# Kernel optimization log

Hardware: AMD Instinct MI355X
Metric: run time of the kernel (lower is better)

## Reference

```python
import jax, jax.numpy as jnp
import numpy as np

I, H, O = 64, 512, 64
B, S = 32, 2048


def setup_inputs() -> dict:
    key = jax.random.key(0)
    ks = jax.random.split(key, 8)
    def xavier(k, shape):
        fan_in, fan_out = shape[1], shape[0]
        lim = jnp.sqrt(6.0 / (fan_in + fan_out))
        return jax.random.uniform(k, shape, jnp.float32, -lim, lim)
    return {
        "x": jax.random.normal(ks[0], (B, S, I), jnp.float32),
        "h_0": jnp.zeros((B, H), jnp.float32),
        "Wz": xavier(ks[1], (H, I + H)),
        "Wr": xavier(ks[2], (H, I + H)),
        "Wh": xavier(ks[3], (H, I + H)),
        "bz": jnp.ones((H,), jnp.float32),
        "br": jnp.zeros((H,), jnp.float32),
        "bh": jnp.zeros((H,), jnp.float32),
        "W1": xavier(ks[4], (H, H)),
        "b1": jnp.zeros((H,), jnp.float32),
        "W2": xavier(ks[5], (O, H)),
        "b2": jnp.zeros((O,), jnp.float32),
    }


def reference(x, h_0, Wz, Wr, Wh, bz, br, bh, W1, b1, W2, b2):
    def step(h_prev, x_t):
        combined = jnp.concatenate([x_t, h_prev], axis=1)          # [B, I+H]
        z = jax.nn.sigmoid(combined @ Wz.T + bz)                   # [B, H]
        r = jax.nn.sigmoid(combined @ Wr.T + br)                   # [B, H]
        gate_input = jnp.concatenate([r * h_prev, x_t], axis=1)    # [B, H+I]
        h_hat = jnp.tanh(gate_input @ Wh.T + bh)                   # [B, H]
        h_t = (1.0 - z) * h_prev + z * h_hat
        out = jax.nn.relu(h_t @ W1.T + b1) @ W2.T + b2             # [B, O]
        return h_t, out

    # scan over time: x -> [S, B, I]
    h_last, outs = jax.lax.scan(step, h_0, jnp.swapaxes(x, 0, 1))
    return jnp.swapaxes(outs, 0, 1), h_last  # [B, S, O], [B, H]
```

## Files before the change

kernel.cpp:

```cpp
#include <hip/hip_runtime.h>
#include <stdint.h>

#define S_LEN 2048
#define NW 16
#define KPAD 584

typedef __attribute__((ext_vector_type(8))) short short8;
typedef __attribute__((ext_vector_type(4))) float f32x4;

__device__ __forceinline__ unsigned short f2bf(float f) {
  union { float f; unsigned int u; } v; v.f = f;
  unsigned int u = v.u;
  u = (u + 0x7FFFu + ((u >> 16) & 1u)) >> 16;
  return (unsigned short)u;
}

__device__ __forceinline__ float sigm(float x) { return 1.f / (1.f + __expf(-x)); }
__device__ __forceinline__ float tanh_f(float x) {
  float e = __expf(2.f * x);
  return 1.f - 2.f / (e + 1.f);
}

__device__ __forceinline__ void group_barrier(unsigned int* p, unsigned int target) {
  __syncthreads();
  if (threadIdx.x == 0) {
    __threadfence();
    __hip_atomic_fetch_add(p, 1u, __ATOMIC_RELEASE, __HIP_MEMORY_SCOPE_AGENT);
    unsigned int it = 0;
    while (__hip_atomic_load(p, __ATOMIC_RELAXED, __HIP_MEMORY_SCOPE_AGENT) < target) {
      __builtin_amdgcn_s_sleep(1);
      if (++it > (1u << 22)) break;
    }
    __threadfence();
  }
  __syncthreads();
}

__global__ void prep_kernel(const float* __restrict__ Wz, const float* __restrict__ Wr,
                            const float* __restrict__ Wh, const float* __restrict__ W1,
                            const float* __restrict__ W2,
                            unsigned short* __restrict__ WgT,
                            unsigned short* __restrict__ W1T,
                            unsigned short* __restrict__ W2T) {
  const int total = 1536 * 576 + 512 * 512 + 64 * 512;
  for (int idx = blockIdx.x * 256 + threadIdx.x; idx < total; idx += gridDim.x * 256) {
    if (idx < 1536 * 576) {
      int row = idx / 576, k = idx % 576;
      float v;
      if (row < 512)       v = Wz[row * 576 + k];
      else if (row < 1024) v = Wr[(row - 512) * 576 + k];
      else {
        int r = row - 1024;
        v = (k < 64) ? Wh[r * 576 + 512 + k] : Wh[r * 576 + (k - 64)];
      }
      WgT[idx] = f2bf(v);
    } else if (idx < 1536 * 576 + 512 * 512) {
      int i = idx - 1536 * 576;
      W1T[i] = f2bf(W1[i]);
    } else {
      int i = idx - 1536 * 576 - 512 * 512;
      W2T[i] = f2bf(W2[i]);
    }
  }
}

__global__ void __launch_bounds__(256, 1) recur_kernel(
    const float* __restrict__ x, const float* __restrict__ h0,
    const float* __restrict__ bz, const float* __restrict__ br,
    const float* __restrict__ bh, const unsigned short* __restrict__ WgT,
    unsigned short* __restrict__ hbuf, unsigned short* __restrict__ rhbuf,
    unsigned short* __restrict__ h_all, float* __restrict__ h_last,
    unsigned int* __restrict__ ctr) {
  extern __shared__ char smem[];
  unsigned short* Wlds = (unsigned short*)smem;
  unsigned short* Abuf = Wlds + 96 * KPAD;
  float* hfp = (float*)(Abuf + 16 * KPAD);

  const int wg = blockIdx.x;
  const int g = wg >> 4;
  const int w = wg & 15;
  const int tid = threadIdx.x;
  const int lane = tid & 63;
  const int wave = tid >> 6;
  const int crow = (lane >> 4) << 2;
  const int ccol = lane & 15;

  for (int i = tid; i < 96 * 72; i += 256) {
    int lr = i / 72, c = i % 72;
    int gate = lr >> 5, col = lr & 31;
    const uint4* src = (const uint4*)(WgT + (size_t)(gate * 512 + w * 32 + col) * 576);
    *(uint4*)(Wlds + lr * KPAD + c * 8) = src[c];
  }
  for (int i = tid; i < 16 * 32; i += 256) {
    int m = i >> 5, c = i & 31;
    hfp[m * 32 + c] = h0[(size_t)(g * 16 + m) * 512 + w * 32 + c];
  }
  __syncthreads();

  unsigned int* myctr = ctr + g * 4096;
  float zreg[4];

  for (int t = 0; t < S_LEN; ++t) {
    {
      int i = tid;
      int m = i >> 4, c4 = i & 15;
      float4 xv = *(const float4*)(x + ((size_t)(g * 16 + m) * S_LEN + t) * 64 + c4 * 4);
      unsigned short* d = Abuf + m * KPAD + c4 * 4;
      d[0] = f2bf(xv.x); d[1] = f2bf(xv.y); d[2] = f2bf(xv.z); d[3] = f2bf(xv.w);
    }
    if (t == 0) {
      for (int i = tid; i < 16 * 128; i += 256) {
        int m = i >> 7, c4 = i & 127;
        float4 hv = *(const float4*)(h0 + (size_t)(g * 16 + m) * 512 + c4 * 4);
        unsigned short* d = Abuf + m * KPAD + 64 + c4 * 4;
        d[0] = f2bf(hv.x); d[1] = f2bf(hv.y); d[2] = f2bf(hv.z); d[3] = f2bf(hv.w);
      }
    } else {
      for (int i = tid; i < 16 * 64; i += 256) {
        int m = i >> 6, c8 = i & 63;
        uint4 v = *(const uint4*)(hbuf + (size_t)(g * 16 + m) * 512 + c8 * 8);
        *(uint4*)(Abuf + m * KPAD + 64 + c8 * 8) = v;
      }
    }
    __syncthreads();

    {
      const int gsel = wave >> 1;
      const int tile = wave & 1;
      const unsigned short* Ap = Abuf + ccol * KPAD + ((lane >> 4) << 3);
      const unsigned short* Bp = Wlds + (gsel * 32 + tile * 16 + ccol) * KPAD + ((lane >> 4) << 3);
      f32x4 acc = {0.f, 0.f, 0.f, 0.f};
#pragma unroll
      for (int kk = 0; kk < 18; ++kk) {
        short8 a = *(const short8*)(Ap + kk * 32);
        short8 b = *(const short8*)(Bp + kk * 32);
        acc = __builtin_amdgcn_mfma_f32_16x16x32_bf16(a, b, acc, 0, 0, 0);
      }
      const int nloc = tile * 16 + ccol;
      const int ng = w * 32 + nloc;
      const float bias = (gsel == 0) ? bz[ng] : br[ng];
      if (gsel == 0) {
#pragma unroll
        for (int j = 0; j < 4; ++j) zreg[j] = sigm(acc[j] + bias);
      } else {
#pragma unroll
        for (int j = 0; j < 4; ++j) {
          int m = crow + j;
          float rv = sigm(acc[j] + bias);
          float rh = rv * hfp[m * 32 + nloc];
          rhbuf[(size_t)(g * 16 + m) * 512 + ng] = f2bf(rh);
        }
      }
    }
    group_barrier(myctr + t * 2, NW);

    for (int i = tid; i < 16 * 64; i += 256) {
      int m = i >> 6, c8 = i & 63;
      uint4 v = *(const uint4*)(rhbuf + (size_t)(g * 16 + m) * 512 + c8 * 8);
      *(uint4*)(Abuf + m * KPAD + 64 + c8 * 8) = v;
    }
    __syncthreads();

    if (wave < 2) {
      const unsigned short* Ap = Abuf + ccol * KPAD + ((lane >> 4) << 3);
      const unsigned short* Bp = Wlds + (64 + wave * 16 + ccol) * KPAD + ((lane >> 4) << 3);
      f32x4 acc = {0.f, 0.f, 0.f, 0.f};
#pragma unroll
      for (int kk = 0; kk < 18; ++kk) {
        short8 a = *(const short8*)(Ap + kk * 32);
        short8 b = *(const short8*)(Bp + kk * 32);
        acc = __builtin_amdgcn_mfma_f32_16x16x32_bf16(a, b, acc, 0, 0, 0);
      }
      const int nloc = wave * 16 + ccol;
      const int ng = w * 32 + nloc;
      const float bias = bh[ng];
#pragma unroll
      for (int j = 0; j < 4; ++j) {
        int m = crow + j;
        float hh = tanh_f(acc[j] + bias);
        float hold = hfp[m * 32 + nloc];
        float z = zreg[j];
        float hn = (1.f - z) * hold + z * hh;
        hfp[m * 32 + nloc] = hn;
        unsigned short hb = f2bf(hn);
        hbuf[(size_t)(g * 16 + m) * 512 + ng] = hb;
        h_all[((size_t)(g * 16 + m) * S_LEN + t) * 512 + ng] = hb;
        if (t == S_LEN - 1) h_last[(size_t)(g * 16 + m) * 512 + ng] = hn;
      }
    }
    group_barrier(myctr + t * 2 + 1, NW);
  }
}

__global__ void __launch_bounds__(256, 1) head_kernel(
    const unsigned short* __restrict__ h_all, const unsigned short* __restrict__ W1T,
    const unsigned short* __restrict__ W2T, const float* __restrict__ b1,
    const float* __restrict__ b2, float* __restrict__ out) {
  extern __shared__ char smem[];
  unsigned short* hs = (unsigned short*)smem;
  unsigned short* act = hs + 64 * 520;

  const int tid = threadIdx.x, lane = tid & 63, wave = tid >> 6;
  const int crow = (lane >> 4) << 2, ccol = lane & 15;
  const size_t row0 = (size_t)blockIdx.x * 64;

  for (int i = tid; i < 64 * 64; i += 256) {
    int r = i >> 6, c8 = i & 63;
    uint4 v = *(const uint4*)(h_all + (row0 + r) * 512 + c8 * 8);
    *(uint4*)(hs + r * 520 + c8 * 8) = v;
  }
  __syncthreads();

  f32x4 acc[8][4];
#pragma unroll
  for (int nt = 0; nt < 8; ++nt)
#pragma unroll
    for (int mt = 0; mt < 4; ++mt) acc[nt][mt] = {0.f, 0.f, 0.f, 0.f};

  for (int k = 0; k < 16; ++k) {
    short8 a[4];
#pragma unroll
    for (int mt = 0; mt < 4; ++mt)
      a[mt] = *(const short8*)(hs + (mt * 16 + ccol) * 520 + k * 32 + ((lane >> 4) << 3));
#pragma unroll
    for (int nt = 0; nt < 8; ++nt) {
      int n0 = (wave * 8 + nt) * 16;
      short8 b = *(const short8*)(W1T + (size_t)(n0 + ccol) * 512 + k * 32 + ((lane >> 4) << 3));
#pragma unroll
      for (int mt = 0; mt < 4; ++mt)
        acc[nt][mt] = __builtin_amdgcn_mfma_f32_16x16x32_bf16(a[mt], b, acc[nt][mt], 0, 0, 0);
    }
  }
#pragma unroll
  for (int nt = 0; nt < 8; ++nt) {
    int n = wave * 128 + nt * 16 + ccol;
    float bias = b1[n];
#pragma unroll
    for (int mt = 0; mt < 4; ++mt)
#pragma unroll
      for (int j = 0; j < 4; ++j) {
        float v = fmaxf(acc[nt][mt][j] + bias, 0.f);
        act[(mt * 16 + crow + j) * 520 + n] = f2bf(v);
      }
  }
  __syncthreads();
  for (int i = tid; i < 64 * 64; i += 256) {
    int r = i >> 6, c8 = i & 63;
    uint4 v = *(const uint4*)(W2T + (size_t)r * 512 + c8 * 8);
    *(uint4*)(hs + r * 520 + c8 * 8) = v;
  }
  __syncthreads();

  f32x4 acc2[4];
#pragma unroll
  for (int nt = 0; nt < 4; ++nt) acc2[nt] = {0.f, 0.f, 0.f, 0.f};
  for (int k = 0; k < 16; ++k) {
    short8 a = *(const short8*)(act + (wave * 16 + ccol) * 520 + k * 32 + ((lane >> 4) << 3));
#pragma unroll
    for (int nt = 0; nt < 4; ++nt) {
      short8 b = *(const short8*)(hs + (nt * 16 + ccol) * 520 + k * 32 + ((lane >> 4) << 3));
      acc2[nt] = __builtin_amdgcn_mfma_f32_16x16x32_bf16(a, b, acc2[nt], 0, 0, 0);
    }
  }
#pragma unroll
  for (int nt = 0; nt < 4; ++nt) {
    int o = nt * 16 + ccol;
    float bias = b2[o];
#pragma unroll
    for (int j = 0; j < 4; ++j) {
      int r = wave * 16 + crow + j;
      out[(row0 + r) * 64 + o] = acc2[nt][j] + bias;
    }
  }
}

extern "C" void kernel_launch(void* const* d_in, const int* in_sizes, int n_in,
                              void* d_out, int out_size, void* d_ws, size_t ws_size,
                              hipStream_t stream) {
  const float* x  = (const float*)d_in[0];
  const float* h0 = (const float*)d_in[1];
  const float* Wz = (const float*)d_in[2];
  const float* Wr = (const float*)d_in[3];
  const float* Wh = (const float*)d_in[4];
  const float* bz = (const float*)d_in[5];
  const float* br = (const float*)d_in[6];
  const float* bh = (const float*)d_in[7];
  const float* W1 = (const float*)d_in[8];
  const float* b1 = (const float*)d_in[9];
  const float* W2 = (const float*)d_in[10];
  const float* b2 = (const float*)d_in[11];

  char* ws = (char*)d_ws;
  size_t off = 0;
  unsigned int*   ctr   = (unsigned int*)(ws + off);   off += 32768;
  unsigned short* hbuf  = (unsigned short*)(ws + off); off += 32 * 512 * 2;
  unsigned short* rhbuf = (unsigned short*)(ws + off); off += 32 * 512 * 2;
  unsigned short* WgT   = (unsigned short*)(ws + off); off += (size_t)1536 * 576 * 2;
  unsigned short* W1T   = (unsigned short*)(ws + off); off += (size_t)512 * 512 * 2;
  unsigned short* W2T   = (unsigned short*)(ws + off); off += (size_t)64 * 512 * 2;
  unsigned short* h_all = (unsigned short*)(ws + off); off += (size_t)32 * 2048 * 512 * 2;

  float* out = (float*)d_out;
  float* h_last = out + (size_t)32 * 2048 * 64;

  hipMemsetAsync(ctr, 0, 32768, stream);
  hipLaunchKernelGGL(prep_kernel, dim3(1024), dim3(256), 0, stream,
                     Wz, Wr, Wh, W1, W2, WgT, W1T, W2T);

  const int recur_lds = (96 * KPAD + 16 * KPAD) * 2 + 16 * 32 * 4;
  hipFuncSetAttribute(reinterpret_cast<const void*>(&recur_kernel),
                      hipFuncAttributeMaxDynamicSharedMemorySize, recur_lds);
  hipLaunchKernelGGL(recur_kernel, dim3(32), dim3(256), recur_lds, stream,
                     x, h0, bz, br, bh, WgT, hbuf, rhbuf, h_all, h_last, ctr);

  const int head_lds = 2 * 64 * 520 * 2;
  hipFuncSetAttribute(reinterpret_cast<const void*>(&head_kernel),
                      hipFuncAttributeMaxDynamicSharedMemorySize, head_lds);
  hipLaunchKernelGGL(head_kernel, dim3(1024), dim3(256), head_lds, stream,
                     h_all, W1T, W2T, b1, b2, out);
}
```

Measured before the change: 19.34 ms.

## Replace atomic-counter barriers with per-workgroup flags and direct global operand loads

The recurrent kernel's group barrier (atomic add, fence, sleep-poll) becomes per-workgroup monotonic flags that one wave polls with a wave-wide all-check, without sleeps or heavy fences. The h and r*h operands are read straight from global memory into registers via relaxed agent-scope atomic loads instead of being staged through LDS. Weights are pre-swizzled into MFMA fragment order in LDS, x for the next step is prefetched and converted during the current step, and the MFMA chain is split into two accumulators. The aim is to cut per-step synchronisation latency on the serial 2048-step critical path. The price is relying on relaxed atomics without explicit fences for cross-workgroup visibility, which is a memory-ordering risk.

```diff
diff --git a/kernel.cpp b/kernel.cpp
--- a/kernel.cpp
+++ b/kernel.cpp
@@ -2,9 +2,8 @@
 #include <stdint.h>
 
 #define S_LEN 2048
-#define NW 16
-#define KPAD 584
-
+
+typedef unsigned long long u64;
 typedef __attribute__((ext_vector_type(8))) short short8;
 typedef __attribute__((ext_vector_type(4))) float f32x4;
 
@@ -15,25 +14,11 @@
   return (unsigned short)u;
 }
 
-__device__ __forceinline__ float sigm(float x) { return 1.f / (1.f + __expf(-x)); }
-__device__ __forceinline__ float tanh_f(float x) {
-  float e = __expf(2.f * x);
-  return 1.f - 2.f / (e + 1.f);
-}
-
-__device__ __forceinline__ void group_barrier(unsigned int* p, unsigned int target) {
-  __syncthreads();
-  if (threadIdx.x == 0) {
-    __threadfence();
-    __hip_atomic_fetch_add(p, 1u, __ATOMIC_RELEASE, __HIP_MEMORY_SCOPE_AGENT);
-    unsigned int it = 0;
-    while (__hip_atomic_load(p, __ATOMIC_RELAXED, __HIP_MEMORY_SCOPE_AGENT) < target) {
-      __builtin_amdgcn_s_sleep(1);
-      if (++it > (1u << 22)) break;
-    }
-    __threadfence();
-  }
-  __syncthreads();
+__device__ __forceinline__ void st_bf(unsigned short* p, unsigned short v) {
+  __hip_atomic_store(p, v, __ATOMIC_RELAXED, __HIP_MEMORY_SCOPE_AGENT);
+}
+__device__ __forceinline__ u64 ld_u64(const unsigned short* p) {
+  return __hip_atomic_load((const u64*)p, __ATOMIC_RELAXED, __HIP_MEMORY_SCOPE_AGENT);
 }
 
 __global__ void prep_kernel(const float* __restrict__ Wz, const float* __restrict__ Wr,
@@ -70,125 +55,170 @@
     const float* __restrict__ bh, const unsigned short* __restrict__ WgT,
     unsigned short* __restrict__ hbuf, unsigned short* __restrict__ rhbuf,
     unsigned short* __restrict__ h_all, float* __restrict__ h_last,
-    unsigned int* __restrict__ ctr) {
+    unsigned int* __restrict__ flags) {
   extern __shared__ char smem[];
-  unsigned short* Wlds = (unsigned short*)smem;
-  unsigned short* Abuf = Wlds + 96 * KPAD;
-  float* hfp = (float*)(Abuf + 16 * KPAD);
+  unsigned short* Wf = (unsigned short*)smem;
+  unsigned short* Xf = Wf + 6 * 18 * 64 * 8;
+  float* hfp = (float*)(Xf + 2 * 64 * 8);
 
   const int wg = blockIdx.x;
-  const int g = wg >> 4;
-  const int w = wg & 15;
+  const int g = wg >> 4, w = wg & 15;
   const int tid = threadIdx.x;
-  const int lane = tid & 63;
-  const int wave = tid >> 6;
+  const int lane = tid & 63, wave = tid >> 6;
   const int crow = (lane >> 4) << 2;
   const int ccol = lane & 15;
-
-  for (int i = tid; i < 96 * 72; i += 256) {
-    int lr = i / 72, c = i % 72;
-    int gate = lr >> 5, col = lr & 31;
-    const uint4* src = (const uint4*)(WgT + (size_t)(gate * 512 + w * 32 + col) * 576);
-    *(uint4*)(Wlds + lr * KPAD + c * 8) = src[c];
-  }
-  for (int i = tid; i < 16 * 32; i += 256) {
+  const int ko8 = (lane >> 4) << 3;
+
+  for (int i = tid; i < 6 * 18 * 64; i += 256) {
+    int T = i / (18 * 64);
+    int kk = (i >> 6) % 18;
+    int l = i & 63;
+    int row = (T >> 1) * 512 + w * 32 + (T & 1) * 16 + (l & 15);
+    int k = kk * 32 + ((l >> 4) << 3);
+    uint4 v = *(const uint4*)(WgT + (size_t)row * 576 + k);
+    *(uint4*)(Wf + (size_t)i * 8) = v;
+  }
+  for (int i = tid; i < 512; i += 256) {
     int m = i >> 5, c = i & 31;
-    hfp[m * 32 + c] = h0[(size_t)(g * 16 + m) * 512 + w * 32 + c];
+    float hv = h0[(size_t)(g * 16 + m) * 512 + w * 32 + c];
+    hfp[m * 32 + c] = hv;
+    st_bf(hbuf + (size_t)(g * 16 + m) * 512 + w * 32 + c, f2bf(hv));
+  }
+  const int pm = tid >> 4, pf4 = tid & 15;
+  float4 xreg = *(const float4*)(x + ((size_t)(g * 16 + pm) * S_LEN + 0) * 64 + pf4 * 4);
+  {
+    int c = pf4 >> 1;
+    int F = (c >> 2) * 64 + (c & 3) * 16 + pm;
+    unsigned short tmp[4] = {f2bf(xreg.x), f2bf(xreg.y), f2bf(xreg.z), f2bf(xreg.w)};
+    *(u64*)(Xf + F * 8 + (pf4 & 1) * 4) = *(u64*)tmp;
   }
   __syncthreads();
 
-  unsigned int* myctr = ctr + g * 4096;
+  unsigned int* myflag = flags + g * 256 + w * 16;
+  const unsigned int* gflags = flags + g * 256;
+  if (tid == 0)
+    __hip_atomic_store(myflag, 1u, __ATOMIC_RELAXED, __HIP_MEMORY_SCOPE_AGENT);
+
+  float bzv = 0.f, brv = 0.f, bhv = 0.f;
+  if (wave < 2) { bzv = bz[w * 32 + wave * 16 + ccol]; bhv = bh[w * 32 + wave * 16 + ccol]; }
+  else          { brv = br[w * 32 + (wave & 1) * 16 + ccol]; }
+
+  const unsigned short* hsrc  = hbuf  + (size_t)(g * 16 + ccol) * 512 + ko8;
+  const unsigned short* rhsrc = rhbuf + (size_t)(g * 16 + ccol) * 512 + ko8;
+
   float zreg[4];
 
   for (int t = 0; t < S_LEN; ++t) {
-    {
-      int i = tid;
-      int m = i >> 4, c4 = i & 15;
-      float4 xv = *(const float4*)(x + ((size_t)(g * 16 + m) * S_LEN + t) * 64 + c4 * 4);
-      unsigned short* d = Abuf + m * KPAD + c4 * 4;
-      d[0] = f2bf(xv.x); d[1] = f2bf(xv.y); d[2] = f2bf(xv.z); d[3] = f2bf(xv.w);
-    }
-    if (t == 0) {
-      for (int i = tid; i < 16 * 128; i += 256) {
-        int m = i >> 7, c4 = i & 127;
-        float4 hv = *(const float4*)(h0 + (size_t)(g * 16 + m) * 512 + c4 * 4);
-        unsigned short* d = Abuf + m * KPAD + 64 + c4 * 4;
-        d[0] = f2bf(hv.x); d[1] = f2bf(hv.y); d[2] = f2bf(hv.z); d[3] = f2bf(hv.w);
-      }
+    if (wave == 0) {
+      const unsigned int* fl = gflags + (lane & 15) * 16;
+      unsigned int it = 0;
+      for (;;) {
+        unsigned int v = __hip_atomic_load(fl, __ATOMIC_RELAXED, __HIP_MEMORY_SCOPE_AGENT);
+        if (__all((int)(v >= (unsigned)(2 * t + 1)))) break;
+        if (++it > (1u << 22)) break;
+      }
+    }
+    __syncthreads();
+
+    short8 aarr[16];
+#pragma unroll
+    for (int kk = 0; kk < 16; ++kk) {
+      union { u64 q[2]; short8 v; } u;
+      u.q[0] = ld_u64(hsrc + kk * 32);
+      u.q[1] = ld_u64(hsrc + kk * 32 + 4);
+      aarr[kk] = u.v;
+    }
+    const unsigned short* Bb = Wf + (size_t)wave * 18 * 512 + lane * 8;
+    short8 ax0 = *(const short8*)(Xf + (0 * 64 + lane) * 8);
+    short8 ax1 = *(const short8*)(Xf + (1 * 64 + lane) * 8);
+    f32x4 acc0 = {0.f, 0.f, 0.f, 0.f}, acc1 = {0.f, 0.f, 0.f, 0.f};
+    acc0 = __builtin_amdgcn_mfma_f32_16x16x32_bf16(ax0, *(const short8*)(Bb + 0 * 512), acc0, 0, 0, 0);
+    acc1 = __builtin_amdgcn_mfma_f32_16x16x32_bf16(ax1, *(const short8*)(Bb + 1 * 512), acc1, 0, 0, 0);
+#pragma unroll
+    for (int kk = 0; kk < 16; kk += 2) {
+      acc0 = __builtin_amdgcn_mfma_f32_16x16x32_bf16(aarr[kk],     *(const short8*)(Bb + (kk + 2) * 512), acc0, 0, 0, 0);
+      acc1 = __builtin_amdgcn_mfma_f32_16x16x32_bf16(aarr[kk + 1], *(const short8*)(Bb + (kk + 3) * 512), acc1, 0, 0, 0);
+    }
+    f32x4 acc = acc0 + acc1;
+    if (wave < 2) {
+#pragma unroll
+      for (int j = 0; j < 4; ++j)
+        zreg[j] = 1.f / (1.f + __expf(-(acc[j] + bzv)));
     } else {
-      for (int i = tid; i < 16 * 64; i += 256) {
-        int m = i >> 6, c8 = i & 63;
-        uint4 v = *(const uint4*)(hbuf + (size_t)(g * 16 + m) * 512 + c8 * 8);
-        *(uint4*)(Abuf + m * KPAD + 64 + c8 * 8) = v;
+      const int nloc = (wave & 1) * 16 + ccol;
+      const int ng = w * 32 + nloc;
+#pragma unroll
+      for (int j = 0; j < 4; ++j) {
+        int m = crow + j;
+        float rv = 1.f / (1.f + __expf(-(acc[j] + brv)));
+        float rh = rv * hfp[m * 32 + nloc];
+        st_bf(rhbuf + (size_t)(g * 16 + m) * 512 + ng, f2bf(rh));
       }
     }
     __syncthreads();
-
-    {
-      const int gsel = wave >> 1;
-      const int tile = wave & 1;
-      const unsigned short* Ap = Abuf + ccol * KPAD + ((lane >> 4) << 3);
-      const unsigned short* Bp = Wlds + (gsel * 32 + tile * 16 + ccol) * KPAD + ((lane >> 4) << 3);
-      f32x4 acc = {0.f, 0.f, 0.f, 0.f};
-#pragma unroll
-      for (int kk = 0; kk < 18; ++kk) {
-        short8 a = *(const short8*)(Ap + kk * 32);
-        short8 b = *(const short8*)(Bp + kk * 32);
-        acc = __builtin_amdgcn_mfma_f32_16x16x32_bf16(a, b, acc, 0, 0, 0);
-      }
-      const int nloc = tile * 16 + ccol;
-      const int ng = w * 32 + nloc;
-      const float bias = (gsel == 0) ? bz[ng] : br[ng];
-      if (gsel == 0) {
-#pragma unroll
-        for (int j = 0; j < 4; ++j) zreg[j] = sigm(acc[j] + bias);
-      } else {
-#pragma unroll
-        for (int j = 0; j < 4; ++j) {
-          int m = crow + j;
-          float rv = sigm(acc[j] + bias);
-          float rh = rv * hfp[m * 32 + nloc];
-          rhbuf[(size_t)(g * 16 + m) * 512 + ng] = f2bf(rh);
-        }
-      }
-    }
-    group_barrier(myctr + t * 2, NW);
-
-    for (int i = tid; i < 16 * 64; i += 256) {
-      int m = i >> 6, c8 = i & 63;
-      uint4 v = *(const uint4*)(rhbuf + (size_t)(g * 16 + m) * 512 + c8 * 8);
-      *(uint4*)(Abuf + m * KPAD + 64 + c8 * 8) = v;
+    if (tid == 0)
+      __hip_atomic_store(myflag, (unsigned)(2 * t + 2), __ATOMIC_RELAXED, __HIP_MEMORY_SCOPE_AGENT);
+
+    if (wave == 0) {
+      const unsigned int* fl = gflags + (lane & 15) * 16;
+      unsigned int it = 0;
+      for (;;) {
+        unsigned int v = __hip_atomic_load(fl, __ATOMIC_RELAXED, __HIP_MEMORY_SCOPE_AGENT);
+        if (__all((int)(v >= (unsigned)(2 * t + 2)))) break;
+        if (++it > (1u << 22)) break;
+      }
     }
     __syncthreads();
 
+    int tn = (t + 1 < S_LEN) ? t + 1 : t;
+    xreg = *(const float4*)(x + ((size_t)(g * 16 + pm) * S_LEN + tn) * 64 + pf4 * 4);
+
     if (wave < 2) {
-      const unsigned short* Ap = Abuf + ccol * KPAD + ((lane >> 4) << 3);
-      const unsigned short* Bp = Wlds + (64 + wave * 16 + ccol) * KPAD + ((lane >> 4) << 3);
-      f32x4 acc = {0.f, 0.f, 0.f, 0.f};
-#pragma unroll
-      for (int kk = 0; kk < 18; ++kk) {
-        short8 a = *(const short8*)(Ap + kk * 32);
-        short8 b = *(const short8*)(Bp + kk * 32);
-        acc = __builtin_amdgcn_mfma_f32_16x16x32_bf16(a, b, acc, 0, 0, 0);
-      }
+      short8 barr[16];
+#pragma unroll
+      for (int kk = 0; kk < 16; ++kk) {
+        union { u64 q[2]; short8 v; } u2;
+        u2.q[0] = ld_u64(rhsrc + kk * 32);
+        u2.q[1] = ld_u64(rhsrc + kk * 32 + 4);
+        barr[kk] = u2.v;
+      }
+      const unsigned short* Bh = Wf + (size_t)(4 + wave) * 18 * 512 + lane * 8;
+      f32x4 b0 = {0.f, 0.f, 0.f, 0.f}, b1 = {0.f, 0.f, 0.f, 0.f};
+      b0 = __builtin_amdgcn_mfma_f32_16x16x32_bf16(ax0, *(const short8*)(Bh + 0 * 512), b0, 0, 0, 0);
+      b1 = __builtin_amdgcn_mfma_f32_16x16x32_bf16(ax1, *(const short8*)(Bh + 1 * 512), b1, 0, 0, 0);
+#pragma unroll
+      for (int kk = 0; kk < 16; kk += 2) {
+        b0 = __builtin_amdgcn_mfma_f32_16x16x32_bf16(barr[kk],     *(const short8*)(Bh + (kk + 2) * 512), b0, 0, 0, 0);
+        b1 = __builtin_amdgcn_mfma_f32_16x16x32_bf16(barr[kk + 1], *(const short8*)(Bh + (kk + 3) * 512), b1, 0, 0, 0);
+      }
+      f32x4 hacc = b0 + b1;
       const int nloc = wave * 16 + ccol;
       const int ng = w * 32 + nloc;
-      const float bias = bh[ng];
 #pragma unroll
       for (int j = 0; j < 4; ++j) {
         int m = crow + j;
-        float hh = tanh_f(acc[j] + bias);
+        float e = __expf(2.f * (hacc[j] + bhv));
+        float hh = 1.f - 2.f / (e + 1.f);
         float hold = hfp[m * 32 + nloc];
         float z = zreg[j];
         float hn = (1.f - z) * hold + z * hh;
         hfp[m * 32 + nloc] = hn;
         unsigned short hb = f2bf(hn);
-        hbuf[(size_t)(g * 16 + m) * 512 + ng] = hb;
+        st_bf(hbuf + (size_t)(g * 16 + m) * 512 + ng, hb);
         h_all[((size_t)(g * 16 + m) * S_LEN + t) * 512 + ng] = hb;
         if (t == S_LEN - 1) h_last[(size_t)(g * 16 + m) * 512 + ng] = hn;
       }
     }
-    group_barrier(myctr + t * 2 + 1, NW);
+    __syncthreads();
+    if (tid == 0)
+      __hip_atomic_store(myflag, (unsigned)(2 * t + 3), __ATOMIC_RELAXED, __HIP_MEMORY_SCOPE_AGENT);
+
+    {
+      int c = pf4 >> 1;
+      int F = (c >> 2) * 64 + (c & 3) * 16 + pm;
+      unsigned short tmp[4] = {f2bf(xreg.x), f2bf(xreg.y), f2bf(xreg.z), f2bf(xreg.w)};
+      *(u64*)(Xf + F * 8 + (pf4 & 1) * 4) = *(u64*)tmp;
+    }
   }
 }
 
@@ -292,7 +322,7 @@
 
   char* ws = (char*)d_ws;
   size_t off = 0;
-  unsigned int*   ctr   = (unsigned int*)(ws + off);   off += 32768;
+  unsigned int*   flags = (unsigned int*)(ws + off);   off += 4096;
   unsigned short* hbuf  = (unsigned short*)(ws + off); off += 32 * 512 * 2;
   unsigned short* rhbuf = (unsigned short*)(ws + off); off += 32 * 512 * 2;
   unsigned short* WgT   = (unsigned short*)(ws + off); off += (size_t)1536 * 576 * 2;
@@ -303,15 +333,15 @@
   float* out = (float*)d_out;
   float* h_last = out + (size_t)32 * 2048 * 64;
 
-  hipMemsetAsync(ctr, 0, 32768, stream);
+  hipMemsetAsync(flags, 0, 4096, stream);
   hipLaunchKernelGGL(prep_kernel, dim3(1024), dim3(256), 0, stream,
                      Wz, Wr, Wh, W1, W2, WgT, W1T, W2T);
 
-  const int recur_lds = (96 * KPAD + 16 * KPAD) * 2 + 16 * 32 * 4;
+  const int recur_lds = (6 * 18 * 64 * 8 + 2 * 64 * 8) * 2 + 16 * 32 * 4;
   hipFuncSetAttribute(reinterpret_cast<const void*>(&recur_kernel),
                       hipFuncAttributeMaxDynamicSharedMemorySize, recur_lds);
   hipLaunchKernelGGL(recur_kernel, dim3(32), dim3(256), recur_lds, stream,
-                     x, h0, bz, br, bh, WgT, hbuf, rhbuf, h_all, h_last, ctr);
+                     x, h0, bz, br, bh, WgT, hbuf, rhbuf, h_all, h_last, flags);
 
   const int head_lds = 2 * 64 * 520 * 2;
   hipFuncSetAttribute(reinterpret_cast<const void*>(&head_kernel),
```

New measurement: 17.06 ms. 1.13x faster.
